# Optimization experiments

Hardware: AMD Instinct MI355X
Metric: run time of the kernel (lower is better)

The kernel has to match this reference:

```python
import jax, jax.numpy as jnp
import numpy as np

FUT_LEN = 12
OBS_LEN = 8
N_COORD = 2
HIDDEN = 128  # z_dim + s_dim = 64 + 64
N_AGENTS = 131072


def setup_inputs() -> dict:
    key = jax.random.key(0)
    ks = jax.random.split(key, 9)
    H, C = HIDDEN, N_COORD
    return {
        "obs_traj_rel": jax.random.normal(ks[0], (OBS_LEN, N_AGENTS, C), jnp.float32),
        "fut_traj_rel": jax.random.normal(ks[1], (FUT_LEN, N_AGENTS, C), jnp.float32),
        "pred_lstm_hidden": jax.random.normal(ks[2], (N_AGENTS, H), jnp.float32),
        # LSTMCell params (PyTorch layout: [4H, in] / [4H, H], gate order i,f,g,o)
        "W_ih": 0.1 * jax.random.normal(ks[3], (4 * H, C), jnp.float32),
        "W_hh": 0.1 * jax.random.normal(ks[4], (4 * H, H), jnp.float32),
        "b_ih": jnp.zeros((4 * H,), jnp.float32),
        "b_hh": jnp.zeros((4 * H,), jnp.float32),
        # hidden2pos Linear
        "W_out": 0.1 * jax.random.normal(ks[5], (C, H), jnp.float32),
        "b_out": jnp.zeros((C,), jnp.float32),
    }


def reference(obs_traj_rel, fut_traj_rel, pred_lstm_hidden,
              W_ih, W_hh, b_ih, b_hh, W_out, b_out):
    H = pred_lstm_hidden.shape[-1]
    x0 = obs_traj_rel[OBS_LEN - 1, :, :N_COORD]           # [N, 2]
    c0 = jnp.zeros_like(pred_lstm_hidden)                  # [N, H]

    def step(carry, _):
        h, c, x = carry
        gates = x @ W_ih.T + b_ih + h @ W_hh.T + b_hh      # [N, 4H]
        i, f, g, o = jnp.split(gates, 4, axis=-1)          # PyTorch gate order
        c_new = jax.nn.sigmoid(f) * c + jax.nn.sigmoid(i) * jnp.tanh(g)
        h_new = jax.nn.sigmoid(o) * jnp.tanh(c_new)
        out = h_new @ W_out.T + b_out                      # [N, 2]
        return (h_new, c_new, out), out

    _, outs = jax.lax.scan(step, (pred_lstm_hidden, c0, x0), None, length=FUT_LEN)
    return outs  # [fut_len, N, 2]
```

## Files before the change

kernel.cpp:

```cpp
#include <hip/hip_runtime.h>

typedef unsigned short u16;
typedef __attribute__((ext_vector_type(8))) short short8;
typedef __attribute__((ext_vector_type(4))) float f32x4;
typedef __attribute__((ext_vector_type(2))) float f32x2;

#define N_AGENTS 131072
#define HID 128
#define FUT 12
#define OBS 8

constexpr int PAIRS = 4;
#define NEG_K  (-1.4426950408889634f)
#define NEG_2K (-2.8853900817779268f)

__device__ __forceinline__ u16 f2bf(float f) {
    union { float f; unsigned int i; } v; v.f = f;
    unsigned int u = v.i;
    return (u16)((u + 0x7fffu + ((u >> 16) & 1u)) >> 16);
}
__device__ __forceinline__ float bexp2(float x) {
#if __has_builtin(__builtin_amdgcn_exp2f)
    return __builtin_amdgcn_exp2f(x);
#else
    float r; asm("v_exp_f32 %0, %1" : "=v"(r) : "v"(x)); return r;
#endif
}
__device__ __forceinline__ float brcp(float x) {
#if __has_builtin(__builtin_amdgcn_rcpf)
    return __builtin_amdgcn_rcpf(x);
#else
    float r; asm("v_rcp_f32 %0, %1" : "=v"(r) : "v"(x)); return r;
#endif
}
__device__ __forceinline__ unsigned cvtpk(float lo, float hi) {
    unsigned r; asm("v_cvt_pk_bf16_f32 %0, %1, %2" : "=v"(r) : "v"(lo), "v"(hi)); return r;
}

__launch_bounds__(512, 2)
__global__ void lstm_dec_kernel(const float* __restrict__ obs,
                                const float* __restrict__ h0g,
                                const float* __restrict__ Wih,
                                const float* __restrict__ Whh,
                                const float* __restrict__ bih,
                                const float* __restrict__ bhh,
                                const float* __restrict__ Wout,
                                const float* __restrict__ bout,
                                float* __restrict__ dout)
{
    __shared__ short8 hb[2][32][17];
    __shared__ float  xt[32][2];
    __shared__ float  ot[FUT][32][2];

    const int tid  = threadIdx.x;
    const int lane = tid & 63;
    const int wv   = tid >> 6;
    const int r    = lane & 15;
    const int kb   = lane >> 4;

    const float bout0 = bout[0];
    const float bout1 = bout[1];

    const float gsc[4] = {NEG_K, NEG_K, NEG_2K, NEG_K};

    float wihs0[4], wihs1[4];
    f32x4 accInit[4];
#pragma unroll
    for (int nt = 0; nt < 4; ++nt) {
        int c = nt * HID + wv * 16 + r;
        float w0 = Wih[c * 2 + 0];
        float w1 = Wih[c * 2 + 1];
        float be = (bih[c] + bhh[c] + w0 * bout0 + w1 * bout1) * gsc[nt];
        wihs0[nt] = w0 * gsc[nt];
        wihs1[nt] = w1 * gsc[nt];
        accInit[nt] = f32x4{be, be, be, be};
    }
    const float bo = (r == 0) ? bout0 : ((r == 1) ? bout1 : 0.0f);
    const f32x4 oInit = {bo, bo, bo, bo};

    short8 bfrag[4][4];
    short8 outb[4];
#pragma unroll
    for (int kf = 0; kf < 4; ++kf) {
        const int k0 = kf * 32 + kb * 8;
        float wo0[8], wo1[8];
        short8 ob;
#pragma unroll
        for (int j = 0; j < 8; ++j) {
            wo0[j] = Wout[0 * HID + k0 + j];
            wo1[j] = Wout[1 * HID + k0 + j];
            float sel = (r == 0) ? wo0[j] : ((r == 1) ? wo1[j] : 0.0f);
            ob[j] = (short)f2bf(sel);
        }
        outb[kf] = ob;
#pragma unroll
        for (int nt = 0; nt < 4; ++nt) {
            int c = nt * HID + wv * 16 + r;
            float s0 = wihs0[nt], s1 = wihs1[nt];
            short8 tt;
#pragma unroll
            for (int j = 0; j < 8; ++j) {
                float f = Whh[(size_t)c * HID + k0 + j] * gsc[nt]
                        + s0 * wo0[j] + s1 * wo1[j];
                tt[j] = (short)f2bf(f);
            }
            bfrag[nt][kf] = tt;
        }
    }

#define LOAD_A(rb)                                                   \
    short8 aA[4], aB[4];                                             \
    _Pragma("unroll")                                                \
    for (int kf = 0; kf < 4; ++kf) {                                 \
        aA[kf] = hb[rb][r][kf * 4 + kb];                             \
        aB[kf] = hb[rb][16 + r][kf * 4 + kb];                        \
    }

#define GATES()                                                      \
    f32x4 accA[4], accB[4];                                          \
    _Pragma("unroll")                                                \
    for (int nt = 0; nt < 4; ++nt) {                                 \
        accA[nt] = __builtin_amdgcn_mfma_f32_16x16x32_bf16(          \
            aA[0], bfrag[nt][0], accInit[nt], 0, 0, 0);              \
        accB[nt] = __builtin_amdgcn_mfma_f32_16x16x32_bf16(          \
            aB[0], bfrag[nt][0], accInit[nt], 0, 0, 0);              \
    }                                                                \
    _Pragma("unroll")                                                \
    for (int kf = 1; kf < 4; ++kf) {                                 \
        _Pragma("unroll")                                            \
        for (int nt = 0; nt < 4; ++nt) {                             \
            accA[nt] = __builtin_amdgcn_mfma_f32_16x16x32_bf16(      \
                aA[kf], bfrag[nt][kf], accA[nt], 0, 0, 0);           \
            accB[nt] = __builtin_amdgcn_mfma_f32_16x16x32_bf16(      \
                aB[kf], bfrag[nt][kf], accB[nt], 0, 0, 0);           \
        }                                                            \
    }

#define OUT_TILE(dst_expr)                                           \
    if (wv == 0) {                                                   \
        f32x4 oacc = __builtin_amdgcn_mfma_f32_16x16x32_bf16(        \
            aA[0], outb[0], oInit, 0, 0, 0);                         \
        _Pragma("unroll")                                            \
        for (int kf = 1; kf < 4; ++kf)                               \
            oacc = __builtin_amdgcn_mfma_f32_16x16x32_bf16(          \
                aA[kf], outb[kf], oacc, 0, 0, 0);                    \
        if (r < 2) {                                                 \
            _Pragma("unroll")                                        \
            for (int q = 0; q < 4; ++q)                              \
                (dst_expr)[kb * 4 + q][r] = oacc[q];                 \
        }                                                            \
    } else if (wv == 1) {                                            \
        f32x4 oacc = __builtin_amdgcn_mfma_f32_16x16x32_bf16(        \
            aB[0], outb[0], oInit, 0, 0, 0);                         \
        _Pragma("unroll")                                            \
        for (int kf = 1; kf < 4; ++kf)                               \
            oacc = __builtin_amdgcn_mfma_f32_16x16x32_bf16(          \
                aB[kf], outb[kf], oacc, 0, 0, 0);                    \
        if (r < 2) {                                                 \
            _Pragma("unroll")                                        \
            for (int q = 0; q < 4; ++q)                              \
                (dst_expr)[16 + kb * 4 + q][r] = oacc[q];            \
        }                                                            \
    }

#define CELL2(q)                                                     \
    {                                                                \
        f32x2 Ei = {bexp2(accA[0][q]), bexp2(accB[0][q])};           \
        f32x2 Ef = {bexp2(accA[1][q]), bexp2(accB[1][q])};           \
        f32x2 Gg = {bexp2(accA[2][q]), bexp2(accB[2][q])};           \
        f32x2 Eo = {bexp2(accA[3][q]), bexp2(accB[3][q])};           \
        f32x2 c2 = {cfA[q], cfB[q]};                                 \
        f32x2 t1 = 1.0f + Ei;                                        \
        f32x2 t2 = 1.0f + Gg;                                        \
        f32x2 t3 = 1.0f + Ef;                                        \
        f32x2 t12 = t1 * t2;                                         \
        f32x2 num = t12 * c2 + t3 * (1.0f - Gg);                     \
        f32x2 den = t12 * t3;                                        \
        f32x2 R1 = {brcp(den.x), brcp(den.y)};                       \
        f32x2 cn = num * R1;                                         \
        cfA[q] = cn.x; cfB[q] = cn.y;                                \
        f32x2 ga = NEG_2K * cn;                                      \
        f32x2 Gc = {bexp2(ga.x), bexp2(ga.y)};                       \
        f32x2 u1 = (1.0f + Eo) * (1.0f + Gc);                        \
        f32x2 R2 = {brcp(u1.x), brcp(u1.y)};                         \
        f32x2 hv = (1.0f - Gc) * R2;                                 \
        unsigned pk = cvtpk(hv.x, hv.y);                             \
        hbase[(kb * 4 + q) * 136 + hcol] = (u16)pk;                  \
        hbase[(16 + kb * 4 + q) * 136 + hcol] = (u16)(pk >> 16);     \
    }

#define ACTIV(wb)                                                    \
    {                                                                \
        u16* hbase = (u16*)&hb[wb][0][0];                            \
        const int hcol = wv * 16 + r;                                \
        CELL2(0) CELL2(1) CELL2(2) CELL2(3)                          \
    }

#pragma unroll 1
    for (int t = 0; t < PAIRS; ++t) {
        const int A0 = (blockIdx.x * PAIRS + t) * 32;

        {
            int row = tid >> 4;
            int c8  = (tid & 15) * 8;
            const float* hp = h0g + (size_t)(A0 + row) * HID + c8;
            f32x4 lo = *(const f32x4*)hp;
            f32x4 hi = *(const f32x4*)(hp + 4);
            short8 a;
            unsigned* ap = (unsigned*)&a;
            ap[0] = cvtpk(lo[0], lo[1]);
            ap[1] = cvtpk(lo[2], lo[3]);
            ap[2] = cvtpk(hi[0], hi[1]);
            ap[3] = cvtpk(hi[2], hi[3]);
            hb[1][row][tid & 15] = a;
        }
        float ox0[8], ox1[8];
#pragma unroll
        for (int hh = 0; hh < 2; ++hh)
#pragma unroll
            for (int q = 0; q < 4; ++q) {
                const float* op = obs + ((size_t)(OBS - 1) * N_AGENTS + A0 + hh * 16 + kb * 4 + q) * 2;
                ox0[hh * 4 + q] = op[0];
                ox1[hh * 4 + q] = op[1];
            }
        f32x4 cfA = {0.f, 0.f, 0.f, 0.f};
        f32x4 cfB = {0.f, 0.f, 0.f, 0.f};
        __syncthreads();

        {
            LOAD_A(1)
            GATES()
            OUT_TILE(xt)
            __syncthreads();
#pragma unroll
            for (int hh = 0; hh < 2; ++hh)
#pragma unroll
                for (int q = 0; q < 4; ++q) {
                    float dx0 = ox0[hh * 4 + q] - xt[hh * 16 + kb * 4 + q][0];
                    float dx1 = ox1[hh * 4 + q] - xt[hh * 16 + kb * 4 + q][1];
#pragma unroll
                    for (int nt = 0; nt < 4; ++nt) {
                        float d = dx0 * wihs0[nt] + dx1 * wihs1[nt];
                        if (hh == 0) accA[nt][q] += d; else accB[nt][q] += d;
                    }
                }
            ACTIV(0)
            __syncthreads();
        }

#pragma unroll 1
        for (int s = 1; s < FUT; ++s) {
            const int rb = (s + 1) & 1;
            LOAD_A(rb)
            GATES()
            OUT_TILE(ot[s - 1])
            ACTIV(s & 1)
            __syncthreads();
        }

        {
            LOAD_A(1)
            OUT_TILE(ot[FUT - 1])
            __syncthreads();
        }

        {
            const float* otf = &ot[0][0][0];
            int idx = tid;
            dout[((size_t)(idx >> 6) * N_AGENTS + A0) * 2 + (idx & 63)] = otf[idx];
            idx = tid + 512;
            if (idx < FUT * 64)
                dout[((size_t)(idx >> 6) * N_AGENTS + A0) * 2 + (idx & 63)] = otf[idx];
        }
    }
#undef LOAD_A
#undef GATES
#undef OUT_TILE
#undef ACTIV
#undef CELL2
}

extern "C" void kernel_launch(void* const* d_in, const int* in_sizes, int n_in,
                              void* d_out, int out_size, void* d_ws, size_t ws_size,
                              hipStream_t stream) {
    const float* obs  = (const float*)d_in[0];
    const float* h0   = (const float*)d_in[2];
    const float* Wih  = (const float*)d_in[3];
    const float* Whh  = (const float*)d_in[4];
    const float* bih  = (const float*)d_in[5];
    const float* bhh  = (const float*)d_in[6];
    const float* Wout = (const float*)d_in[7];
    const float* bo   = (const float*)d_in[8];
    float* out = (float*)d_out;

    dim3 grid(N_AGENTS / (PAIRS * 32));
    lstm_dec_kernel<<<grid, 512, 0, stream>>>(obs, h0, Wih, Whh, bih, bhh, Wout, bo, out);
}
```

Measured before the change: 295.3 us.

## Software-pipeline LSTM halves so one half's MFMA overlaps the other's activations

Splits each 32-agent tile into two 16-row halves (A and B) and staggers them. Each phase now issues the gate MFMAs for one half while the sigmoid/tanh activation work for the other half is computed, so matrix and vector ALU work can interleave within a wave. The cost is twice as many barriers per time step, extra prologue and epilogue phases, and a loop unrolled by two, which may raise register pressure and code size.

Measured after the change: 300.1 us. Within noise of the previous version (+1.6%).

```diff
diff --git a/kernel.cpp b/kernel.cpp
--- a/kernel.cpp
+++ b/kernel.cpp
@@ -108,68 +108,45 @@
         }
     }
 
-#define LOAD_A(rb)                                                   \
-    short8 aA[4], aB[4];                                             \
+#define LOADF(a, rb, rowoff)                                         \
     _Pragma("unroll")                                                \
-    for (int kf = 0; kf < 4; ++kf) {                                 \
-        aA[kf] = hb[rb][r][kf * 4 + kb];                             \
-        aB[kf] = hb[rb][16 + r][kf * 4 + kb];                        \
-    }
-
-#define GATES()                                                      \
-    f32x4 accA[4], accB[4];                                          \
+    for (int kf = 0; kf < 4; ++kf)                                   \
+        a[kf] = hb[rb][(rowoff) + r][kf * 4 + kb];
+
+#define GATES_ONE(acc, a)                                            \
     _Pragma("unroll")                                                \
-    for (int nt = 0; nt < 4; ++nt) {                                 \
-        accA[nt] = __builtin_amdgcn_mfma_f32_16x16x32_bf16(          \
-            aA[0], bfrag[nt][0], accInit[nt], 0, 0, 0);              \
-        accB[nt] = __builtin_amdgcn_mfma_f32_16x16x32_bf16(          \
-            aB[0], bfrag[nt][0], accInit[nt], 0, 0, 0);              \
-    }                                                                \
+    for (int nt = 0; nt < 4; ++nt)                                   \
+        acc[nt] = __builtin_amdgcn_mfma_f32_16x16x32_bf16(           \
+            a[0], bfrag[nt][0], accInit[nt], 0, 0, 0);               \
     _Pragma("unroll")                                                \
-    for (int kf = 1; kf < 4; ++kf) {                                 \
+    for (int kf = 1; kf < 4; ++kf)                                   \
         _Pragma("unroll")                                            \
-        for (int nt = 0; nt < 4; ++nt) {                             \
-            accA[nt] = __builtin_amdgcn_mfma_f32_16x16x32_bf16(      \
-                aA[kf], bfrag[nt][kf], accA[nt], 0, 0, 0);           \
-            accB[nt] = __builtin_amdgcn_mfma_f32_16x16x32_bf16(      \
-                aB[kf], bfrag[nt][kf], accB[nt], 0, 0, 0);           \
-        }                                                            \
-    }
-
-#define OUT_TILE(dst_expr)                                           \
-    if (wv == 0) {                                                   \
+        for (int nt = 0; nt < 4; ++nt)                               \
+            acc[nt] = __builtin_amdgcn_mfma_f32_16x16x32_bf16(       \
+                a[kf], bfrag[nt][kf], acc[nt], 0, 0, 0);
+
+#define OUT_ONE(whichwv, a, dst_expr, rowoff)                        \
+    if (wv == (whichwv)) {                                           \
         f32x4 oacc = __builtin_amdgcn_mfma_f32_16x16x32_bf16(        \
-            aA[0], outb[0], oInit, 0, 0, 0);                         \
+            a[0], outb[0], oInit, 0, 0, 0);                          \
         _Pragma("unroll")                                            \
         for (int kf = 1; kf < 4; ++kf)                               \
             oacc = __builtin_amdgcn_mfma_f32_16x16x32_bf16(          \
-                aA[kf], outb[kf], oacc, 0, 0, 0);                    \
+                a[kf], outb[kf], oacc, 0, 0, 0);                     \
         if (r < 2) {                                                 \
             _Pragma("unroll")                                        \
             for (int q = 0; q < 4; ++q)                              \
-                (dst_expr)[kb * 4 + q][r] = oacc[q];                 \
+                (dst_expr)[(rowoff) + kb * 4 + q][r] = oacc[q];      \
         }                                                            \
-    } else if (wv == 1) {                                            \
-        f32x4 oacc = __builtin_amdgcn_mfma_f32_16x16x32_bf16(        \
-            aB[0], outb[0], oInit, 0, 0, 0);                         \
-        _Pragma("unroll")                                            \
-        for (int kf = 1; kf < 4; ++kf)                               \
-            oacc = __builtin_amdgcn_mfma_f32_16x16x32_bf16(          \
-                aB[kf], outb[kf], oacc, 0, 0, 0);                    \
-        if (r < 2) {                                                 \
-            _Pragma("unroll")                                        \
-            for (int q = 0; q < 4; ++q)                              \
-                (dst_expr)[16 + kb * 4 + q][r] = oacc[q];            \
-        }                                                            \
-    }
-
-#define CELL2(q)                                                     \
+    }
+
+#define CELLP(acc, cf, qa, qb, rowoff)                               \
     {                                                                \
-        f32x2 Ei = {bexp2(accA[0][q]), bexp2(accB[0][q])};           \
-        f32x2 Ef = {bexp2(accA[1][q]), bexp2(accB[1][q])};           \
-        f32x2 Gg = {bexp2(accA[2][q]), bexp2(accB[2][q])};           \
-        f32x2 Eo = {bexp2(accA[3][q]), bexp2(accB[3][q])};           \
-        f32x2 c2 = {cfA[q], cfB[q]};                                 \
+        f32x2 Ei = {bexp2(acc[0][qa]), bexp2(acc[0][qb])};           \
+        f32x2 Ef = {bexp2(acc[1][qa]), bexp2(acc[1][qb])};           \
+        f32x2 Gg = {bexp2(acc[2][qa]), bexp2(acc[2][qb])};           \
+        f32x2 Eo = {bexp2(acc[3][qa]), bexp2(acc[3][qb])};           \
+        f32x2 c2 = {cf[qa], cf[qb]};                                 \
         f32x2 t1 = 1.0f + Ei;                                        \
         f32x2 t2 = 1.0f + Gg;                                        \
         f32x2 t3 = 1.0f + Ef;                                        \
@@ -178,22 +155,33 @@
         f32x2 den = t12 * t3;                                        \
         f32x2 R1 = {brcp(den.x), brcp(den.y)};                       \
         f32x2 cn = num * R1;                                         \
-        cfA[q] = cn.x; cfB[q] = cn.y;                                \
+        cf[qa] = cn.x; cf[qb] = cn.y;                                \
         f32x2 ga = NEG_2K * cn;                                      \
         f32x2 Gc = {bexp2(ga.x), bexp2(ga.y)};                       \
         f32x2 u1 = (1.0f + Eo) * (1.0f + Gc);                        \
         f32x2 R2 = {brcp(u1.x), brcp(u1.y)};                         \
         f32x2 hv = (1.0f - Gc) * R2;                                 \
         unsigned pk = cvtpk(hv.x, hv.y);                             \
-        hbase[(kb * 4 + q) * 136 + hcol] = (u16)pk;                  \
-        hbase[(16 + kb * 4 + q) * 136 + hcol] = (u16)(pk >> 16);     \
-    }
-
-#define ACTIV(wb)                                                    \
+        hbase[((rowoff) + kb * 4 + qa) * 136 + hcol] = (u16)pk;      \
+        hbase[((rowoff) + kb * 4 + qb) * 136 + hcol] = (u16)(pk >> 16); \
+    }
+
+#define ACTIV_ONE(acc, cf, wb, rowoff)                               \
     {                                                                \
         u16* hbase = (u16*)&hb[wb][0][0];                            \
         const int hcol = wv * 16 + r;                                \
-        CELL2(0) CELL2(1) CELL2(2) CELL2(3)                          \
+        CELLP(acc, cf, 0, 1, rowoff)                                 \
+        CELLP(acc, cf, 2, 3, rowoff)                                 \
+    }
+
+#define CORR(acc, ox0v, ox1v, rowoff)                                \
+    _Pragma("unroll")                                                \
+    for (int q = 0; q < 4; ++q) {                                    \
+        float dx0 = ox0v[q] - xt[(rowoff) + kb * 4 + q][0];          \
+        float dx1 = ox1v[q] - xt[(rowoff) + kb * 4 + q][1];          \
+        _Pragma("unroll")                                            \
+        for (int nt = 0; nt < 4; ++nt)                               \
+            acc[nt][q] += dx0 * wihs0[nt] + dx1 * wihs1[nt];         \
     }
 
 #pragma unroll 1
@@ -214,55 +202,74 @@
             ap[3] = cvtpk(hi[2], hi[3]);
             hb[1][row][tid & 15] = a;
         }
-        float ox0[8], ox1[8];
-#pragma unroll
-        for (int hh = 0; hh < 2; ++hh)
-#pragma unroll
-            for (int q = 0; q < 4; ++q) {
-                const float* op = obs + ((size_t)(OBS - 1) * N_AGENTS + A0 + hh * 16 + kb * 4 + q) * 2;
-                ox0[hh * 4 + q] = op[0];
-                ox1[hh * 4 + q] = op[1];
-            }
+        float oxA0[4], oxA1[4], oxB0[4], oxB1[4];
+#pragma unroll
+        for (int q = 0; q < 4; ++q) {
+            const float* opA = obs + ((size_t)(OBS - 1) * N_AGENTS + A0 + kb * 4 + q) * 2;
+            const float* opB = obs + ((size_t)(OBS - 1) * N_AGENTS + A0 + 16 + kb * 4 + q) * 2;
+            oxA0[q] = opA[0]; oxA1[q] = opA[1];
+            oxB0[q] = opB[0]; oxB1[q] = opB[1];
+        }
         f32x4 cfA = {0.f, 0.f, 0.f, 0.f};
         f32x4 cfB = {0.f, 0.f, 0.f, 0.f};
-        __syncthreads();
-
-        {
-            LOAD_A(1)
-            GATES()
-            OUT_TILE(xt)
+        f32x4 accA[4], accB[4];
+        __syncthreads();
+
+        {
+            short8 aA[4];
+            LOADF(aA, 1, 0)
+            GATES_ONE(accA, aA)
+            OUT_ONE(0, aA, xt, 0)
+        }
+        __syncthreads();
+
+        {
+            short8 aB[4];
+            LOADF(aB, 1, 16)
+            GATES_ONE(accB, aB)
+            OUT_ONE(1, aB, xt, 16)
+            CORR(accA, oxA0, oxA1, 0)
+            ACTIV_ONE(accA, cfA, 0, 0)
+        }
+        __syncthreads();
+
+#pragma unroll 2
+        for (int s = 1; s < FUT; ++s) {
+            const int rp = (s - 1) & 1;
+            const int wp = s & 1;
+            {
+                short8 aA[4];
+                LOADF(aA, rp, 0)
+                GATES_ONE(accA, aA)
+                OUT_ONE(0, aA, ot[s - 1], 0)
+                if (s == 1) { CORR(accB, oxB0, oxB1, 16) }
+                ACTIV_ONE(accB, cfB, rp, 16)
+            }
             __syncthreads();
-#pragma unroll
-            for (int hh = 0; hh < 2; ++hh)
-#pragma unroll
-                for (int q = 0; q < 4; ++q) {
-                    float dx0 = ox0[hh * 4 + q] - xt[hh * 16 + kb * 4 + q][0];
-                    float dx1 = ox1[hh * 4 + q] - xt[hh * 16 + kb * 4 + q][1];
-#pragma unroll
-                    for (int nt = 0; nt < 4; ++nt) {
-                        float d = dx0 * wihs0[nt] + dx1 * wihs1[nt];
-                        if (hh == 0) accA[nt][q] += d; else accB[nt][q] += d;
-                    }
-                }
-            ACTIV(0)
+            {
+                short8 aB[4];
+                LOADF(aB, rp, 16)
+                GATES_ONE(accB, aB)
+                OUT_ONE(1, aB, ot[s - 1], 16)
+                ACTIV_ONE(accA, cfA, wp, 0)
+            }
             __syncthreads();
         }
 
-#pragma unroll 1
-        for (int s = 1; s < FUT; ++s) {
-            const int rb = (s + 1) & 1;
-            LOAD_A(rb)
-            GATES()
-            OUT_TILE(ot[s - 1])
-            ACTIV(s & 1)
-            __syncthreads();
-        }
-
-        {
-            LOAD_A(1)
-            OUT_TILE(ot[FUT - 1])
-            __syncthreads();
-        }
+        {
+            short8 aA[4];
+            LOADF(aA, 1, 0)
+            OUT_ONE(0, aA, ot[FUT - 1], 0)
+            ACTIV_ONE(accB, cfB, 1, 16)
+        }
+        __syncthreads();
+
+        {
+            short8 aB[4];
+            LOADF(aB, 1, 16)
+            OUT_ONE(1, aB, ot[FUT - 1], 16)
+        }
+        __syncthreads();
 
         {
             const float* otf = &ot[0][0][0];
@@ -273,11 +280,12 @@
                 dout[((size_t)(idx >> 6) * N_AGENTS + A0) * 2 + (idx & 63)] = otf[idx];
         }
     }
-#undef LOAD_A
-#undef GATES
-#undef OUT_TILE
-#undef ACTIV
-#undef CELL2
+#undef LOADF
+#undef GATES_ONE
+#undef OUT_ONE
+#undef CELLP
+#undef ACTIV_ONE
+#undef CORR
 }
 
 extern "C" void kernel_launch(void* const* d_in, const int* in_sizes, int n_in,
```

## Remap LSTM work to 256-thread blocks with 16 agents and 8 column tiles per wave

Applied to the files above, without the earlier changes.

Shrinks the block from 512 to 256 threads and from 32 to 16 agents per tile. Each wave now covers two 64-column slices of the gate matrix, keeping 32 bf16 weight fragments in registers, while one set of A fragments is shared across both slices. The bias is added after the MFMA instead of serving as the accumulator init. The output-projection weights move to LDS, and outputs are written straight to global memory each step instead of being staged in shared memory. This is meant to raise MFMA work per A-fragment load and cut LDS traffic, at the cost of much higher register pressure, uncoalesced per-step output stores, and Wih reloads in the correction step.

Result: slower. 379.9 us (+28.7%).

```diff
diff --git a/kernel.cpp b/kernel.cpp
--- a/kernel.cpp
+++ b/kernel.cpp
@@ -10,7 +10,7 @@
 #define FUT 12
 #define OBS 8
 
-constexpr int PAIRS = 4;
+constexpr int AG = 8;
 #define NEG_K  (-1.4426950408889634f)
 #define NEG_2K (-2.8853900817779268f)
 
@@ -37,7 +37,7 @@
     unsigned r; asm("v_cvt_pk_bf16_f32 %0, %1, %2" : "=v"(r) : "v"(lo), "v"(hi)); return r;
 }
 
-__launch_bounds__(512, 2)
+__launch_bounds__(256, 2)
 __global__ void lstm_dec_kernel(const float* __restrict__ obs,
                                 const float* __restrict__ h0g,
                                 const float* __restrict__ Wih,
@@ -48,9 +48,10 @@
                                 const float* __restrict__ bout,
                                 float* __restrict__ dout)
 {
-    __shared__ short8 hb[2][32][17];
-    __shared__ float  xt[32][2];
-    __shared__ float  ot[FUT][32][2];
+    __shared__ short8 hb[2][16][17];
+    __shared__ float  xt[16][2];
+    __shared__ float  obs_s[32];
+    __shared__ short8 outb_lds[4][64];
 
     const int tid  = threadIdx.x;
     const int lane = tid & 63;
@@ -61,115 +62,131 @@
     const float bout0 = bout[0];
     const float bout1 = bout[1];
 
-    const float gsc[4] = {NEG_K, NEG_K, NEG_2K, NEG_K};
-
-    float wihs0[4], wihs1[4];
-    f32x4 accInit[4];
-#pragma unroll
-    for (int nt = 0; nt < 4; ++nt) {
-        int c = nt * HID + wv * 16 + r;
-        float w0 = Wih[c * 2 + 0];
-        float w1 = Wih[c * 2 + 1];
-        float be = (bih[c] + bhh[c] + w0 * bout0 + w1 * bout1) * gsc[nt];
-        wihs0[nt] = w0 * gsc[nt];
-        wihs1[nt] = w1 * gsc[nt];
-        accInit[nt] = f32x4{be, be, be, be};
-    }
-    const float bo = (r == 0) ? bout0 : ((r == 1) ? bout1 : 0.0f);
-    const f32x4 oInit = {bo, bo, bo, bo};
-
-    short8 bfrag[4][4];
-    short8 outb[4];
+    const float gscn[4] = {NEG_K, NEG_K, NEG_2K, NEG_K};
+
+    float beff[2][4];
+#pragma unroll
+    for (int ct = 0; ct < 2; ++ct)
+#pragma unroll
+        for (int nt = 0; nt < 4; ++nt) {
+            int c = nt * HID + ct * 64 + wv * 16 + r;
+            float w0 = Wih[c * 2 + 0];
+            float w1 = Wih[c * 2 + 1];
+            beff[ct][nt] = (bih[c] + bhh[c] + w0 * bout0 + w1 * bout1) * gscn[nt];
+        }
+
+    short8 bfrag[2][4][4];
 #pragma unroll
     for (int kf = 0; kf < 4; ++kf) {
         const int k0 = kf * 32 + kb * 8;
         float wo0[8], wo1[8];
-        short8 ob;
 #pragma unroll
         for (int j = 0; j < 8; ++j) {
             wo0[j] = Wout[0 * HID + k0 + j];
             wo1[j] = Wout[1 * HID + k0 + j];
-            float sel = (r == 0) ? wo0[j] : ((r == 1) ? wo1[j] : 0.0f);
-            ob[j] = (short)f2bf(sel);
-        }
-        outb[kf] = ob;
-#pragma unroll
-        for (int nt = 0; nt < 4; ++nt) {
-            int c = nt * HID + wv * 16 + r;
-            float s0 = wihs0[nt], s1 = wihs1[nt];
-            short8 tt;
+        }
+        if (wv == 0) {
+            short8 ob;
 #pragma unroll
             for (int j = 0; j < 8; ++j) {
-                float f = Whh[(size_t)c * HID + k0 + j] * gsc[nt]
-                        + s0 * wo0[j] + s1 * wo1[j];
-                tt[j] = (short)f2bf(f);
+                float sel = (r == 0) ? wo0[j] : ((r == 1) ? wo1[j] : 0.0f);
+                ob[j] = (short)f2bf(sel);
             }
-            bfrag[nt][kf] = tt;
-        }
-    }
-
-#define LOAD_A(rb)                                                   \
-    short8 aA[4], aB[4];                                             \
+            outb_lds[kf][lane] = ob;
+        }
+#pragma unroll
+        for (int ct = 0; ct < 2; ++ct)
+#pragma unroll
+            for (int nt = 0; nt < 4; ++nt) {
+                int c = nt * HID + ct * 64 + wv * 16 + r;
+                float s0 = Wih[c * 2 + 0] * gscn[nt];
+                float s1 = Wih[c * 2 + 1] * gscn[nt];
+                short8 tt;
+#pragma unroll
+                for (int j = 0; j < 8; ++j) {
+                    float f = Whh[(size_t)c * HID + k0 + j] * gscn[nt]
+                            + s0 * wo0[j] + s1 * wo1[j];
+                    tt[j] = (short)f2bf(f);
+                }
+                bfrag[ct][nt][kf] = tt;
+            }
+    }
+
+#define LOADF(rb)                                                    \
     _Pragma("unroll")                                                \
-    for (int kf = 0; kf < 4; ++kf) {                                 \
-        aA[kf] = hb[rb][r][kf * 4 + kb];                             \
-        aB[kf] = hb[rb][16 + r][kf * 4 + kb];                        \
-    }
+    for (int kf = 0; kf < 4; ++kf)                                   \
+        af[kf] = hb[rb][r][kf * 4 + kb];
 
 #define GATES()                                                      \
-    f32x4 accA[4], accB[4];                                          \
-    _Pragma("unroll")                                                \
-    for (int nt = 0; nt < 4; ++nt) {                                 \
-        accA[nt] = __builtin_amdgcn_mfma_f32_16x16x32_bf16(          \
-            aA[0], bfrag[nt][0], accInit[nt], 0, 0, 0);              \
-        accB[nt] = __builtin_amdgcn_mfma_f32_16x16x32_bf16(          \
-            aB[0], bfrag[nt][0], accInit[nt], 0, 0, 0);              \
-    }                                                                \
-    _Pragma("unroll")                                                \
-    for (int kf = 1; kf < 4; ++kf) {                                 \
-        _Pragma("unroll")                                            \
-        for (int nt = 0; nt < 4; ++nt) {                             \
-            accA[nt] = __builtin_amdgcn_mfma_f32_16x16x32_bf16(      \
-                aA[kf], bfrag[nt][kf], accA[nt], 0, 0, 0);           \
-            accB[nt] = __builtin_amdgcn_mfma_f32_16x16x32_bf16(      \
-                aB[kf], bfrag[nt][kf], accB[nt], 0, 0, 0);           \
-        }                                                            \
-    }
-
-#define OUT_TILE(dst_expr)                                           \
+    {                                                                \
+        const f32x4 z4 = {0.f, 0.f, 0.f, 0.f};                       \
+        _Pragma("unroll")                                            \
+        for (int ct = 0; ct < 2; ++ct)                               \
+            _Pragma("unroll")                                        \
+            for (int nt = 0; nt < 4; ++nt)                           \
+                acc[ct][nt] = __builtin_amdgcn_mfma_f32_16x16x32_bf16( \
+                    af[0], bfrag[ct][nt][0], z4, 0, 0, 0);           \
+        _Pragma("unroll")                                            \
+        for (int kf = 1; kf < 4; ++kf)                               \
+            _Pragma("unroll")                                        \
+            for (int ct = 0; ct < 2; ++ct)                           \
+                _Pragma("unroll")                                    \
+                for (int nt = 0; nt < 4; ++nt)                       \
+                    acc[ct][nt] = __builtin_amdgcn_mfma_f32_16x16x32_bf16( \
+                        af[kf], bfrag[ct][nt][kf], acc[ct][nt], 0, 0, 0); \
+    }
+
+#define OUT_TILE(S)                                                  \
     if (wv == 0) {                                                   \
+        const f32x4 z4o = {0.f, 0.f, 0.f, 0.f};                      \
         f32x4 oacc = __builtin_amdgcn_mfma_f32_16x16x32_bf16(        \
-            aA[0], outb[0], oInit, 0, 0, 0);                         \
+            af[0], outb_lds[0][lane], z4o, 0, 0, 0);                 \
         _Pragma("unroll")                                            \
         for (int kf = 1; kf < 4; ++kf)                               \
             oacc = __builtin_amdgcn_mfma_f32_16x16x32_bf16(          \
-                aA[kf], outb[kf], oacc, 0, 0, 0);                    \
+                af[kf], outb_lds[kf][lane], oacc, 0, 0, 0);          \
         if (r < 2) {                                                 \
+            const float bo = (r == 0) ? bout0 : bout1;               \
+            if ((S) == 0) {                                          \
+                _Pragma("unroll")                                    \
+                for (int q = 0; q < 4; ++q)                          \
+                    xt[kb * 4 + q][r] = oacc[q] + bo;                \
+            } else {                                                 \
+                _Pragma("unroll")                                    \
+                for (int q = 0; q < 4; ++q)                          \
+                    dout[((size_t)((S) - 1) * N_AGENTS + A0 + kb * 4 + q) * 2 + r] = oacc[q] + bo; \
+            }                                                        \
+        }                                                            \
+    }
+
+#define CORR()                                                       \
+    {                                                                \
+        float dx0[4], dx1[4];                                        \
+        _Pragma("unroll")                                            \
+        for (int q = 0; q < 4; ++q) {                                \
+            dx0[q] = obs_s[(kb * 4 + q) * 2 + 0] - xt[kb * 4 + q][0]; \
+            dx1[q] = obs_s[(kb * 4 + q) * 2 + 1] - xt[kb * 4 + q][1]; \
+        }                                                            \
+        _Pragma("unroll")                                            \
+        for (int ct = 0; ct < 2; ++ct)                               \
             _Pragma("unroll")                                        \
-            for (int q = 0; q < 4; ++q)                              \
-                (dst_expr)[kb * 4 + q][r] = oacc[q];                 \
-        }                                                            \
-    } else if (wv == 1) {                                            \
-        f32x4 oacc = __builtin_amdgcn_mfma_f32_16x16x32_bf16(        \
-            aB[0], outb[0], oInit, 0, 0, 0);                         \
-        _Pragma("unroll")                                            \
-        for (int kf = 1; kf < 4; ++kf)                               \
-            oacc = __builtin_amdgcn_mfma_f32_16x16x32_bf16(          \
-                aB[kf], outb[kf], oacc, 0, 0, 0);                    \
-        if (r < 2) {                                                 \
-            _Pragma("unroll")                                        \
-            for (int q = 0; q < 4; ++q)                              \
-                (dst_expr)[16 + kb * 4 + q][r] = oacc[q];            \
-        }                                                            \
-    }
-
-#define CELL2(q)                                                     \
-    {                                                                \
-        f32x2 Ei = {bexp2(accA[0][q]), bexp2(accB[0][q])};           \
-        f32x2 Ef = {bexp2(accA[1][q]), bexp2(accB[1][q])};           \
-        f32x2 Gg = {bexp2(accA[2][q]), bexp2(accB[2][q])};           \
-        f32x2 Eo = {bexp2(accA[3][q]), bexp2(accB[3][q])};           \
-        f32x2 c2 = {cfA[q], cfB[q]};                                 \
+            for (int nt = 0; nt < 4; ++nt) {                         \
+                int c = nt * HID + ct * 64 + wv * 16 + r;            \
+                float w0s = Wih[c * 2 + 0] * gscn[nt];               \
+                float w1s = Wih[c * 2 + 1] * gscn[nt];               \
+                _Pragma("unroll")                                    \
+                for (int q = 0; q < 4; ++q)                          \
+                    acc[ct][nt][q] += dx0[q] * w0s + dx1[q] * w1s;   \
+            }                                                        \
+    }
+
+#define CELLP(q)                                                     \
+    {                                                                \
+        f32x2 Ei = {bexp2(acc[0][0][q] + beff[0][0]), bexp2(acc[1][0][q] + beff[1][0])}; \
+        f32x2 Ef = {bexp2(acc[0][1][q] + beff[0][1]), bexp2(acc[1][1][q] + beff[1][1])}; \
+        f32x2 Gg = {bexp2(acc[0][2][q] + beff[0][2]), bexp2(acc[1][2][q] + beff[1][2])}; \
+        f32x2 Eo = {bexp2(acc[0][3][q] + beff[0][3]), bexp2(acc[1][3][q] + beff[1][3])}; \
+        f32x2 c2 = {cf0[q], cf1[q]};                                 \
         f32x2 t1 = 1.0f + Ei;                                        \
         f32x2 t2 = 1.0f + Gg;                                        \
         f32x2 t3 = 1.0f + Ef;                                        \
@@ -178,27 +195,26 @@
         f32x2 den = t12 * t3;                                        \
         f32x2 R1 = {brcp(den.x), brcp(den.y)};                       \
         f32x2 cn = num * R1;                                         \
-        cfA[q] = cn.x; cfB[q] = cn.y;                                \
+        cf0[q] = cn.x; cf1[q] = cn.y;                                \
         f32x2 ga = NEG_2K * cn;                                      \
         f32x2 Gc = {bexp2(ga.x), bexp2(ga.y)};                       \
         f32x2 u1 = (1.0f + Eo) * (1.0f + Gc);                        \
         f32x2 R2 = {brcp(u1.x), brcp(u1.y)};                         \
         f32x2 hv = (1.0f - Gc) * R2;                                 \
         unsigned pk = cvtpk(hv.x, hv.y);                             \
-        hbase[(kb * 4 + q) * 136 + hcol] = (u16)pk;                  \
-        hbase[(16 + kb * 4 + q) * 136 + hcol] = (u16)(pk >> 16);     \
+        hbase[(kb * 4 + q) * 136 + wv * 16 + r] = (u16)pk;           \
+        hbase[(kb * 4 + q) * 136 + 64 + wv * 16 + r] = (u16)(pk >> 16); \
     }
 
 #define ACTIV(wb)                                                    \
     {                                                                \
         u16* hbase = (u16*)&hb[wb][0][0];                            \
-        const int hcol = wv * 16 + r;                                \
-        CELL2(0) CELL2(1) CELL2(2) CELL2(3)                          \
+        CELLP(0) CELLP(1) CELLP(2) CELLP(3)                          \
     }
 
 #pragma unroll 1
-    for (int t = 0; t < PAIRS; ++t) {
-        const int A0 = (blockIdx.x * PAIRS + t) * 32;
+    for (int t = 0; t < AG; ++t) {
+        const int A0 = (blockIdx.x * AG + t) * 16;
 
         {
             int row = tid >> 4;
@@ -214,70 +230,42 @@
             ap[3] = cvtpk(hi[2], hi[3]);
             hb[1][row][tid & 15] = a;
         }
-        float ox0[8], ox1[8];
-#pragma unroll
-        for (int hh = 0; hh < 2; ++hh)
-#pragma unroll
-            for (int q = 0; q < 4; ++q) {
-                const float* op = obs + ((size_t)(OBS - 1) * N_AGENTS + A0 + hh * 16 + kb * 4 + q) * 2;
-                ox0[hh * 4 + q] = op[0];
-                ox1[hh * 4 + q] = op[1];
-            }
-        f32x4 cfA = {0.f, 0.f, 0.f, 0.f};
-        f32x4 cfB = {0.f, 0.f, 0.f, 0.f};
-        __syncthreads();
-
-        {
-            LOAD_A(1)
-            GATES()
-            OUT_TILE(xt)
-            __syncthreads();
-#pragma unroll
-            for (int hh = 0; hh < 2; ++hh)
-#pragma unroll
-                for (int q = 0; q < 4; ++q) {
-                    float dx0 = ox0[hh * 4 + q] - xt[hh * 16 + kb * 4 + q][0];
-                    float dx1 = ox1[hh * 4 + q] - xt[hh * 16 + kb * 4 + q][1];
-#pragma unroll
-                    for (int nt = 0; nt < 4; ++nt) {
-                        float d = dx0 * wihs0[nt] + dx1 * wihs1[nt];
-                        if (hh == 0) accA[nt][q] += d; else accB[nt][q] += d;
-                    }
-                }
-            ACTIV(0)
-            __syncthreads();
-        }
+        if (tid < 32)
+            obs_s[tid] = obs[((size_t)(OBS - 1) * N_AGENTS + A0) * 2 + tid];
+
+        f32x4 cf0 = {0.f, 0.f, 0.f, 0.f};
+        f32x4 cf1 = {0.f, 0.f, 0.f, 0.f};
+        f32x4 acc[2][4];
+        short8 af[4];
+        __syncthreads();
+
+        LOADF(1)
+        GATES()
+        OUT_TILE(0)
+        __syncthreads();
+        CORR()
+        ACTIV(0)
+        __syncthreads();
 
 #pragma unroll 1
         for (int s = 1; s < FUT; ++s) {
-            const int rb = (s + 1) & 1;
-            LOAD_A(rb)
+            LOADF((s - 1) & 1)
             GATES()
-            OUT_TILE(ot[s - 1])
+            OUT_TILE(s)
             ACTIV(s & 1)
             __syncthreads();
         }
 
-        {
-            LOAD_A(1)
-            OUT_TILE(ot[FUT - 1])
-            __syncthreads();
-        }
-
-        {
-            const float* otf = &ot[0][0][0];
-            int idx = tid;
-            dout[((size_t)(idx >> 6) * N_AGENTS + A0) * 2 + (idx & 63)] = otf[idx];
-            idx = tid + 512;
-            if (idx < FUT * 64)
-                dout[((size_t)(idx >> 6) * N_AGENTS + A0) * 2 + (idx & 63)] = otf[idx];
-        }
-    }
-#undef LOAD_A
+        LOADF(1)
+        OUT_TILE(FUT)
+        __syncthreads();
+    }
+#undef LOADF
 #undef GATES
 #undef OUT_TILE
+#undef CORR
+#undef CELLP
 #undef ACTIV
-#undef CELL2
 }
 
 extern "C" void kernel_launch(void* const* d_in, const int* in_sizes, int n_in,
@@ -293,6 +281,6 @@
     const float* bo   = (const float*)d_in[8];
     float* out = (float*)d_out;
 
-    dim3 grid(N_AGENTS / (PAIRS * 32));
-    lstm_dec_kernel<<<grid, 512, 0, stream>>>(obs, h0, Wih, Whh, bih, bhh, Wout, bo, out);
-}
+    dim3 grid(N_AGENTS / (AG * 16));
+    lstm_dec_kernel<<<grid, 256, 0, stream>>>(obs, h0, Wih, Whh, bih, bhh, Wout, bo, out);
+}
```
